# Performance work log

Measured on AMD Instinct MI355X. Metric: run time of the kernel, lower is better.

Reference implementation:

```python
import jax, jax.numpy as jnp
import numpy as np

B, D, E, H, DEPTH, NH, K = 4, 384, 8, 1536, 12, 6, 2
P, NTOK = 16, 197  # patch size, 14*14 patches + cls
EPS = 1e-6


def layernorm(x, w, b):
    m = x.mean(-1, keepdims=True)
    v = ((x - m) ** 2).mean(-1, keepdims=True)
    return (x - m) / jnp.sqrt(v + EPS) * w + b


def attention(x, qkv_w, qkv_b, proj_w, proj_b):
    Bn, N, C = x.shape
    hd = C // NH
    qkv = x @ qkv_w.T + qkv_b                       # [B,N,3C]
    qkv = qkv.reshape(Bn, N, 3, NH, hd).transpose(2, 0, 3, 1, 4)
    q, k, v = qkv[0], qkv[1], qkv[2]                # [B,h,N,hd]
    attn = jax.nn.softmax((q @ k.transpose(0, 1, 3, 2)) * (hd ** -0.5), axis=-1)
    out = (attn @ v).transpose(0, 2, 1, 3).reshape(Bn, N, C)
    return out @ proj_w.T + proj_b


def mlp(x, w1, b1, w2, b2):
    h = jax.nn.gelu(x @ w1.T + b1, approximate=False)
    return h @ w2.T + b2


def moe_ffn(x2d, gw, w1, b1, w2, b2):
    # noiseless top-k gating (eval mode of NoisyTopKGating)
    logits = x2d @ gw                                # [T,E]
    T = logits.shape[0]
    top_vals, top_idx = jax.lax.top_k(logits, K + 1)
    gates_k = jax.nn.softmax(top_vals[:, :K], axis=-1)
    gates = jnp.zeros((T, E), x2d.dtype).at[jnp.arange(T)[:, None], top_idx[:, :K]].set(gates_k)
    # dense per-expert FFN, weighted combine (identical math to SparseDispatcher)
    h = jax.nn.gelu(jnp.einsum('td,edh->teh', x2d, w1) + b1, approximate=False)
    out = jnp.einsum('teh,ehd->ted', h, w2) + b2
    return jnp.einsum('te,ted->td', gates, out)


def forward(x, patch_w, patch_b, cls_token, pos_embed,
            ln1_w, ln1_b, qkv_w, qkv_b, proj_w, proj_b, ln2_w, ln2_b,
            fc1_w, fc1_b, fc2_w, fc2_b,
            gate_w, moe_w1, moe_b1, moe_w2, moe_b2, lnf_w, lnf_b):
    # patch embed: conv k=16 s=16
    feat = jax.lax.conv_general_dilated(x, patch_w, (P, P), 'VALID',
                                        dimension_numbers=('NCHW', 'OIHW', 'NCHW'))
    feat = feat + patch_b[None, :, None, None]
    Bn = feat.shape[0]
    tokens = feat.reshape(Bn, D, -1).transpose(0, 2, 1)          # [B,196,D]
    cls = jnp.broadcast_to(cls_token, (Bn, 1, D))
    h = jnp.concatenate([cls, tokens], axis=1) + pos_embed       # [B,197,D]

    for i in range(DEPTH):
        h = h + attention(layernorm(h, ln1_w[i], ln1_b[i]), qkv_w[i], qkv_b[i], proj_w[i], proj_b[i])
        y = layernorm(h, ln2_w[i], ln2_b[i])
        if i % 2 == 1:
            j = i // 2
            y2 = moe_ffn(y.reshape(-1, D), gate_w[j], moe_w1[j], moe_b1[j], moe_w2[j], moe_b2[j])
            h = h + y2.reshape(Bn, NTOK, D)
        else:
            j = i // 2
            h = h + mlp(y, fc1_w[j], fc1_b[j], fc2_w[j], fc2_b[j])
    return layernorm(h, lnf_w, lnf_b)


def setup_inputs() -> dict:
    key = jax.random.key(0)
    ks = jax.random.split(key, 16)
    rn = lambda k, s, sd=0.02: jax.random.normal(k, s, jnp.float32) * sd
    return {
        'x': jax.random.normal(ks[0], (B, 3, 224, 224), jnp.float32),
        'patch_w': rn(ks[1], (D, 3, P, P)), 'patch_b': jnp.zeros((D,), jnp.float32),
        'cls_token': rn(ks[2], (1, 1, D)), 'pos_embed': rn(ks[3], (1, NTOK, D)),
        'ln1_w': jnp.ones((DEPTH, D), jnp.float32), 'ln1_b': jnp.zeros((DEPTH, D), jnp.float32),
        'qkv_w': rn(ks[4], (DEPTH, 3 * D, D)), 'qkv_b': jnp.zeros((DEPTH, 3 * D), jnp.float32),
        'proj_w': rn(ks[5], (DEPTH, D, D)), 'proj_b': jnp.zeros((DEPTH, D), jnp.float32),
        'ln2_w': jnp.ones((DEPTH, D), jnp.float32), 'ln2_b': jnp.zeros((DEPTH, D), jnp.float32),
        'fc1_w': rn(ks[6], (DEPTH // 2, H, D)), 'fc1_b': jnp.zeros((DEPTH // 2, H), jnp.float32),
        'fc2_w': rn(ks[7], (DEPTH // 2, D, H)), 'fc2_b': jnp.zeros((DEPTH // 2, D), jnp.float32),
        'gate_w': rn(ks[8], (DEPTH // 2, D, E)),
        'moe_w1': rn(ks[9], (DEPTH // 2, E, D, H)), 'moe_b1': jnp.zeros((DEPTH // 2, E, H), jnp.float32),
        'moe_w2': rn(ks[10], (DEPTH // 2, E, H, D)), 'moe_b2': jnp.zeros((DEPTH // 2, E, D), jnp.float32),
        'lnf_w': jnp.ones((D,), jnp.float32), 'lnf_b': jnp.zeros((D,), jnp.float32),
    }


def reference(x, patch_w, patch_b, cls_token, pos_embed,
              ln1_w, ln1_b, qkv_w, qkv_b, proj_w, proj_b, ln2_w, ln2_b,
              fc1_w, fc1_b, fc2_w, fc2_b,
              gate_w, moe_w1, moe_b1, moe_w2, moe_b2, lnf_w, lnf_b):
    return forward(x, patch_w, patch_b, cls_token, pos_embed,
                   ln1_w, ln1_b, qkv_w, qkv_b, proj_w, proj_b, ln2_w, ln2_b,
                   fc1_w, fc1_b, fc2_w, fc2_b,
                   gate_w, moe_w1, moe_b1, moe_w2, moe_b2, lnf_w, lnf_b)
```

## Files before the change

### kernel.cpp

```cpp
#include <hip/hip_runtime.h>
#include <math.h>

#define NBATCH 4
#define NTOK 197
#define TT 788
#define DM 384
#define HM 1536
#define NHEAD 6
#define NEXP 8
#define LD2 72
#define MOUTSZ (TT * 2 * DM)

typedef __attribute__((ext_vector_type(8))) short bf16x8;
typedef __attribute__((ext_vector_type(4))) float f32x4;

__device__ __forceinline__ void f2bf2(float x, short& hi, short& lo) {
    unsigned u = __float_as_uint(x);
    unsigned uh = u + (0x7fffu + ((u >> 16) & 1u));
    hi = (short)(uh >> 16);
    float hf = __uint_as_float(uh & 0xffff0000u);
    float r = x - hf;
    unsigned v = __float_as_uint(r);
    lo = (short)((v + (0x7fffu + ((v >> 16) & 1u))) >> 16);
}
__device__ __forceinline__ float gelu_f(float x) {
    return 0.5f * x * (1.0f + erff(x * 0.7071067811865475f));
}

__global__ void k_im2col(const float* __restrict__ X, float* __restrict__ P) {
    int p = blockIdx.x;
    int b = p / 196, pp = p % 196;
    int py = pp / 14, px = pp % 14;
    const float* xb = X + (size_t)b * 3 * 224 * 224;
    float* dst = P + (size_t)p * 768;
    for (int idx = threadIdx.x; idx < 768; idx += 256) {
        int c = idx >> 8;
        int i = (idx >> 4) & 15;
        int j = idx & 15;
        dst[idx] = xb[((size_t)c * 224 + py * 16 + i) * 224 + px * 16 + j];
    }
}

__global__ void k_assemble(const float* __restrict__ PO, const float* __restrict__ pb,
                           const float* __restrict__ cls, const float* __restrict__ pos,
                           float* __restrict__ H) {
    int t = blockIdx.x;
    int b = t / NTOK, n = t % NTOK;
    for (int d = threadIdx.x; d < DM; d += 128) {
        float v;
        if (n == 0) v = cls[d];
        else v = PO[((size_t)b * 196 + (n - 1)) * DM + d] + pb[d];
        H[(size_t)t * DM + d] = v + pos[(size_t)n * DM + d];
    }
}

__global__ void k_ln(const float* __restrict__ X, const float* __restrict__ w,
                     const float* __restrict__ b, float* __restrict__ Y) {
    int t = blockIdx.x, lane = threadIdx.x;
    const float* x = X + (size_t)t * DM;
    float v[6];
    float s = 0.f;
    #pragma unroll
    for (int i = 0; i < 6; ++i) { v[i] = x[lane + i * 64]; s += v[i]; }
    #pragma unroll
    for (int off = 32; off; off >>= 1) s += __shfl_xor(s, off);
    float mean = s * (1.f / 384.f);
    float q = 0.f;
    #pragma unroll
    for (int i = 0; i < 6; ++i) { float d = v[i] - mean; q += d * d; }
    #pragma unroll
    for (int off = 32; off; off >>= 1) q += __shfl_xor(q, off);
    float inv = rsqrtf(q * (1.f / 384.f) + 1e-6f);
    float* y = Y + (size_t)t * DM;
    #pragma unroll
    for (int i = 0; i < 6; ++i) {
        int d = lane + i * 64;
        y[d] = (v[i] - mean) * inv * w[d] + b[d];
    }
}

__global__ __launch_bounds__(256) void k_gemm_mfma(
    const float* __restrict__ A, const float* __restrict__ W,
    const float* __restrict__ bias, float* __restrict__ C,
    int M, int N, int K, int flags, int MT, int NT, int wprot,
    const float* __restrict__ lnw, const float* __restrict__ lnb)
{
    int mt, nt;
    {
        int lane8 = blockIdx.x & 7;
        int idx = blockIdx.x >> 3;
        if (wprot) {
            mt = idx % MT;
            nt = lane8 + 8 * (idx / MT);
            if (nt >= NT) return;
        } else {
            nt = idx % NT;
            mt = lane8 + 8 * (idx / NT);
            if (mt >= MT) return;
        }
    }
    __shared__ short Ah[64 * LD2], Al[64 * LD2], Bh[64 * LD2], Bl[64 * LD2];
    const int bm = mt * 64, bn = nt * 64;
    const int tid = threadIdx.x;
    const int lane = tid & 63, w = tid >> 6;
    const int wr = w >> 1, wc = w & 1;
    const int r16 = lane & 15, g = lane >> 4;
    const int sr = tid >> 4;
    const int sc = (tid & 15) * 4;
    const bool doln = (flags & 8) != 0;
    float am[4], ai[4];
    #pragma unroll
    for (int p = 0; p < 4; ++p) { am[p] = 0.f; ai[p] = 1.f; }
    if (doln) {
        int j = tid & 15;
        #pragma unroll
        for (int p = 0; p < 4; ++p) {
            int r = bm + sr + p * 16;
            if (r < M) {
                const float* xr = A + (size_t)r * K;
                float s = 0.f, ss = 0.f;
                #pragma unroll
                for (int i = 0; i < 6; ++i) {
                    float4 v = *(const float4*)(xr + j * 4 + i * 64);
                    s += v.x + v.y + v.z + v.w;
                    ss += v.x * v.x + v.y * v.y + v.z * v.z + v.w * v.w;
                }
                #pragma unroll
                for (int off = 1; off < 16; off <<= 1) {
                    s += __shfl_xor(s, off);
                    ss += __shfl_xor(ss, off);
                }
                float mean = s * (1.f / 384.f);
                float var = ss * (1.f / 384.f) - mean * mean;
                am[p] = mean;
                ai[p] = rsqrtf(var + 1e-6f);
            }
        }
    }
    float4 ra[4], rb[4], lw4, lb4;
    auto LOADT = [&](int k0) {
        if (doln) {
            lw4 = *(const float4*)(lnw + k0 + sc);
            lb4 = *(const float4*)(lnb + k0 + sc);
        }
        #pragma unroll
        for (int p = 0; p < 4; ++p) {
            int r = sr + p * 16;
            ra[p] = make_float4(0.f, 0.f, 0.f, 0.f);
            if (bm + r < M) ra[p] = *(const float4*)(A + (size_t)(bm + r) * K + k0 + sc);
            rb[p] = *(const float4*)(W + (size_t)(bn + r) * K + k0 + sc);
        }
    };
    auto STORET = [&]() {
        #pragma unroll
        for (int p = 0; p < 4; ++p) {
            int r = sr + p * 16;
            float4 a4 = ra[p];
            if (doln) {
                a4.x = (a4.x - am[p]) * ai[p] * lw4.x + lb4.x;
                a4.y = (a4.y - am[p]) * ai[p] * lw4.y + lb4.y;
                a4.z = (a4.z - am[p]) * ai[p] * lw4.z + lb4.z;
                a4.w = (a4.w - am[p]) * ai[p] * lw4.w + lb4.w;
            }
            float4 b4 = rb[p];
            short4 ah, al, bh, bl;
            f2bf2(a4.x, ah.x, al.x); f2bf2(a4.y, ah.y, al.y);
            f2bf2(a4.z, ah.z, al.z); f2bf2(a4.w, ah.w, al.w);
            f2bf2(b4.x, bh.x, bl.x); f2bf2(b4.y, bh.y, bl.y);
            f2bf2(b4.z, bh.z, bl.z); f2bf2(b4.w, bh.w, bl.w);
            *(short4*)&Ah[r * LD2 + sc] = ah; *(short4*)&Al[r * LD2 + sc] = al;
            *(short4*)&Bh[r * LD2 + sc] = bh; *(short4*)&Bl[r * LD2 + sc] = bl;
        }
    };
    f32x4 acc[2][2] = {};
    auto COMPUTE = [&]() {
        #pragma unroll
        for (int kk = 0; kk < 2; ++kk) {
            bf16x8 afh[2], afl[2], bfh[2], bfl[2];
            #pragma unroll
            for (int i = 0; i < 2; ++i) {
                int off = (wr * 32 + i * 16 + r16) * LD2 + kk * 32 + g * 8;
                afh[i] = *(const bf16x8*)&Ah[off];
                afl[i] = *(const bf16x8*)&Al[off];
            }
            #pragma unroll
            for (int j = 0; j < 2; ++j) {
                int off = (wc * 32 + j * 16 + r16) * LD2 + kk * 32 + g * 8;
                bfh[j] = *(const bf16x8*)&Bh[off];
                bfl[j] = *(const bf16x8*)&Bl[off];
            }
            #pragma unroll
            for (int i = 0; i < 2; ++i)
                #pragma unroll
                for (int j = 0; j < 2; ++j) {
                    acc[i][j] = __builtin_amdgcn_mfma_f32_16x16x32_bf16(afl[i], bfh[j], acc[i][j], 0, 0, 0);
                    acc[i][j] = __builtin_amdgcn_mfma_f32_16x16x32_bf16(afh[i], bfl[j], acc[i][j], 0, 0, 0);
                    acc[i][j] = __builtin_amdgcn_mfma_f32_16x16x32_bf16(afh[i], bfh[j], acc[i][j], 0, 0, 0);
                }
        }
    };
    LOADT(0);
    STORET();
    __syncthreads();
    for (int k0 = 64; k0 < K; k0 += 64) {
        LOADT(k0);
        COMPUTE();
        __syncthreads();
        STORET();
        __syncthreads();
    }
    COMPUTE();
    #pragma unroll
    for (int i = 0; i < 2; ++i) {
        #pragma unroll
        for (int j = 0; j < 2; ++j) {
            int n = bn + wc * 32 + j * 16 + r16;
            float bb = bias ? bias[n] : 0.f;
            int mbase = bm + wr * 32 + i * 16 + g * 4;
            #pragma unroll
            for (int r = 0; r < 4; ++r) {
                int m = mbase + r;
                if (m < M) {
                    float v = acc[i][j][r] + bb;
                    if (flags & 1) v = gelu_f(v);
                    float* cp = C + (size_t)m * N + n;
                    if (flags & 2) v += *cp;
                    *cp = v;
                }
            }
        }
    }
}

__global__ __launch_bounds__(256) void k_scoresm(const float* __restrict__ QKV,
                                                 float* __restrict__ S) {
    int z = blockIdx.y;
    int b = z / NHEAD, hh = z % NHEAD;
    int i0 = blockIdx.x * 32;
    __shared__ float qs[32][65];
    __shared__ float ks[32][65];
    __shared__ float srow[32][200];
    int tid = threadIdx.x;
    int r = tid >> 3, d0 = (tid & 7) * 8, c0 = (tid & 7) * 4, l8 = tid & 7;
    {
        float4 v0 = make_float4(0,0,0,0), v1 = v0;
        if (i0 + r < NTOK) {
            const float* qp = QKV + ((size_t)(b * NTOK + i0 + r)) * 1152 + hh * 64 + d0;
            v0 = *(const float4*)qp; v1 = *(const float4*)(qp + 4);
        }
        qs[r][d0+0]=v0.x; qs[r][d0+1]=v0.y; qs[r][d0+2]=v0.z; qs[r][d0+3]=v0.w;
        qs[r][d0+4]=v1.x; qs[r][d0+5]=v1.y; qs[r][d0+6]=v1.z; qs[r][d0+7]=v1.w;
    }
    if (l8 == 0) { srow[r][197] = -1e30f; srow[r][198] = -1e30f; srow[r][199] = -1e30f; }
    for (int j0 = 0; j0 < NTOK; j0 += 32) {
        __syncthreads();
        {
            float4 v0 = make_float4(0,0,0,0), v1 = v0;
            if (j0 + r < NTOK) {
                const float* kp = QKV + ((size_t)(b * NTOK + j0 + r)) * 1152 + 384 + hh * 64 + d0;
                v0 = *(const float4*)kp; v1 = *(const float4*)(kp + 4);
            }
            ks[r][d0+0]=v0.x; ks[r][d0+1]=v0.y; ks[r][d0+2]=v0.z; ks[r][d0+3]=v0.w;
            ks[r][d0+4]=v1.x; ks[r][d0+5]=v1.y; ks[r][d0+6]=v1.z; ks[r][d0+7]=v1.w;
        }
        __syncthreads();
        float acc[4] = {0.f, 0.f, 0.f, 0.f};
        #pragma unroll 8
        for (int d = 0; d < 64; ++d) {
            float qv = qs[r][d];
            #pragma unroll
            for (int u = 0; u < 4; ++u) acc[u] += qv * ks[c0 + u][d];
        }
        #pragma unroll
        for (int u = 0; u < 4; ++u) {
            int j = j0 + c0 + u;
            if (j < NTOK) srow[r][j] = acc[u] * 0.125f;
        }
    }
    __syncthreads();
    float m = -1e30f;
    for (int c = l8; c < 200; c += 8) m = fmaxf(m, srow[r][c]);
    #pragma unroll
    for (int off = 1; off < 8; off <<= 1) m = fmaxf(m, __shfl_xor(m, off));
    float s = 0.f;
    for (int c = l8; c < 200; c += 8) {
        float e = expf(srow[r][c] - m);
        srow[r][c] = e;
        s += e;
    }
    #pragma unroll
    for (int off = 1; off < 8; off <<= 1) s += __shfl_xor(s, off);
    float invs = 1.f / s;
    int i = i0 + r;
    if (i < NTOK) {
        float* sp = S + ((size_t)z * NTOK + i) * NTOK;
        for (int c = l8; c < NTOK; c += 8) sp[c] = srow[r][c] * invs;
    }
}

__global__ __launch_bounds__(256) void k_pv(const float* __restrict__ S, const float* __restrict__ QKV,
                                            float* __restrict__ AO) {
    int z = blockIdx.y;
    int b = z / NHEAD, hh = z % NHEAD;
    int i0 = blockIdx.x * 32;
    __shared__ float ps[32][33];
    __shared__ float vs[32][65];
    int tid = threadIdx.x;
    int r = tid >> 3;
    int c4 = (tid & 7) * 4;
    int d0 = (tid & 7) * 8;
    float acc[8] = {};
    for (int k0 = 0; k0 < NTOK; k0 += 32) {
        #pragma unroll
        for (int u = 0; u < 4; ++u) {
            int i = i0 + r, j = k0 + c4 + u;
            ps[r][c4 + u] = (i < NTOK && j < NTOK) ? S[((size_t)z * NTOK + i) * NTOK + j] : 0.f;
        }
        {
            float4 v0 = make_float4(0,0,0,0), v1 = v0;
            if (k0 + r < NTOK) {
                const float* vp = QKV + ((size_t)(b * NTOK + k0 + r)) * 1152 + 768 + hh * 64 + d0;
                v0 = *(const float4*)vp; v1 = *(const float4*)(vp + 4);
            }
            vs[r][d0+0]=v0.x; vs[r][d0+1]=v0.y; vs[r][d0+2]=v0.z; vs[r][d0+3]=v0.w;
            vs[r][d0+4]=v1.x; vs[r][d0+5]=v1.y; vs[r][d0+6]=v1.z; vs[r][d0+7]=v1.w;
        }
        __syncthreads();
        #pragma unroll 8
        for (int kk = 0; kk < 32; ++kk) {
            float pw = ps[r][kk];
            #pragma unroll
            for (int j = 0; j < 8; ++j) acc[j] += pw * vs[kk][d0 + j];
        }
        __syncthreads();
    }
    int i = i0 + r;
    if (i < NTOK) {
        float* op = AO + (size_t)(b * NTOK + i) * DM + hh * 64 + d0;
        #pragma unroll
        for (int j = 0; j < 8; ++j) op[j] = acc[j];
    }
}

__global__ void k_route_ln(const float* __restrict__ H, float* __restrict__ lnstat,
                           const float* __restrict__ lnw, const float* __restrict__ lnb,
                           const float* __restrict__ GW,
                           int* __restrict__ eidx, float* __restrict__ egate) {
    int t = blockIdx.x * 4 + (threadIdx.x >> 6);
    if (t >= TT) return;
    int lane = threadIdx.x & 63;
    const float* x = H + (size_t)t * DM;
    float v[6];
    float s = 0.f, ss = 0.f;
    #pragma unroll
    for (int i = 0; i < 6; ++i) {
        v[i] = x[lane + i * 64];
        s += v[i];
        ss += v[i] * v[i];
    }
    #pragma unroll
    for (int off = 32; off; off >>= 1) { s += __shfl_xor(s, off); ss += __shfl_xor(ss, off); }
    float mean = s * (1.f / 384.f);
    float var = ss * (1.f / 384.f) - mean * mean;
    float inv = rsqrtf(var + 1e-6f);
    if (lane == 0) { lnstat[2 * t] = mean; lnstat[2 * t + 1] = inv; }
    float l8[NEXP] = {};
    #pragma unroll
    for (int i = 0; i < 6; ++i) {
        int d = lane + i * 64;
        float yv = (v[i] - mean) * inv * lnw[d] + lnb[d];
        const float* g = GW + (size_t)d * NEXP;
        #pragma unroll
        for (int e = 0; e < NEXP; ++e) l8[e] += yv * g[e];
    }
    #pragma unroll
    for (int e = 0; e < NEXP; ++e) {
        float vv = l8[e];
        #pragma unroll
        for (int off = 32; off; off >>= 1) vv += __shfl_xor(vv, off);
        l8[e] = vv;
    }
    if (lane == 0) {
        int b0 = 0;
        #pragma unroll
        for (int e = 1; e < NEXP; ++e) if (l8[e] > l8[b0]) b0 = e;
        int b1 = -1;
        #pragma unroll
        for (int e = 0; e < NEXP; ++e) if (e != b0 && (b1 < 0 || l8[e] > l8[b1])) b1 = e;
        float e1 = expf(l8[b1] - l8[b0]);
        float denom = 1.f + e1;
        eidx[2 * t] = b0; eidx[2 * t + 1] = b1;
        egate[2 * t] = 1.f / denom; egate[2 * t + 1] = e1 / denom;
    }
}

__global__ void k_pscatter(int* __restrict__ cnt, int* __restrict__ basep,
                           const int* __restrict__ eidx,
                           int* __restrict__ slot_tok, int* __restrict__ slot_of) {
    __shared__ int hist[NEXP];
    __shared__ int bp[NEXP];
    __shared__ int fl[NEXP];
    int tid = threadIdx.x;
    if (tid < NEXP) { hist[tid] = 0; fl[tid] = 0; }
    __syncthreads();
    for (int i = tid; i < 2 * TT; i += 256) atomicAdd(&hist[eidx[i]], 1);
    __syncthreads();
    if (tid == 0) {
        int s = 0;
        for (int e = 0; e < NEXP; ++e) { bp[e] = s; s += hist[e]; }
    }
    __syncthreads();
    if (tid < NEXP) { cnt[tid] = hist[tid]; basep[tid] = bp[tid]; }
    for (int t = tid; t < TT; t += 256) {
        #pragma unroll
        for (int k = 0; k < 2; ++k) {
            int e = eidx[2 * t + k];
            int pos = atomicAdd(&fl[e], 1);
            int s = bp[e] + pos;
            slot_tok[s] = t;
            slot_of[2 * t + k] = s;
        }
    }
}

__global__ __launch_bounds__(256) void k_moe1_mfma(
    const float* __restrict__ H, const float* __restrict__ lnstat,
    const float* __restrict__ lnw, const float* __restrict__ lnb,
    const float* __restrict__ W1, const float* __restrict__ B1,
    const int* __restrict__ slot_tok, const int* __restrict__ cnt, const int* __restrict__ basep,
    float* __restrict__ HID)
{
    const int e = blockIdx.x & 7;
    const int idx = blockIdx.x >> 3;
    const int mt = idx % 25;
    const int nt = idx / 25;
    const int c = cnt[e];
    const int r0 = mt * 64;
    if (r0 >= c) return;
    const int sbase = basep[e];
    const int n0 = nt * 64;
    const float* W = W1 + (size_t)e * DM * HM;
    const float* B1e = B1 + (size_t)e * HM;
    __shared__ short Ah[64 * LD2], Al[64 * LD2], Bh[64 * LD2], Bl[64 * LD2];
    const int tid = threadIdx.x;
    const int lane = tid & 63, w = tid >> 6;
    const int wr = w >> 1, wc = w & 1;
    const int r16 = lane & 15, g = lane >> 4;
    const int sr = tid >> 4, sc = (tid & 15) * 4;
    const int kq = (tid >> 4) * 4;
    int tokp[4];
    float am4[4], ai4[4];
    #pragma unroll
    for (int p = 0; p < 4; ++p) {
        int m = r0 + sr + p * 16;
        tokp[p] = (m < c) ? slot_tok[sbase + m] : -1;
        am4[p] = 0.f; ai4[p] = 1.f;
        if (tokp[p] >= 0) { am4[p] = lnstat[2 * tokp[p]]; ai4[p] = lnstat[2 * tokp[p] + 1]; }
    }
    f32x4 acc[2][2] = {};
    for (int k0 = 0; k0 < DM; k0 += 64) {
        float4 lw4 = *(const float4*)(lnw + k0 + sc);
        float4 lb4 = *(const float4*)(lnb + k0 + sc);
        #pragma unroll
        for (int p = 0; p < 4; ++p) {
            int r = sr + p * 16;
            float4 a4 = make_float4(0.f, 0.f, 0.f, 0.f);
            if (tokp[p] >= 0) {
                a4 = *(const float4*)(H + (size_t)tokp[p] * DM + k0 + sc);
                a4.x = (a4.x - am4[p]) * ai4[p] * lw4.x + lb4.x;
                a4.y = (a4.y - am4[p]) * ai4[p] * lw4.y + lb4.y;
                a4.z = (a4.z - am4[p]) * ai4[p] * lw4.z + lb4.z;
                a4.w = (a4.w - am4[p]) * ai4[p] * lw4.w + lb4.w;
            }
            short4 ah, al;
            f2bf2(a4.x, ah.x, al.x); f2bf2(a4.y, ah.y, al.y);
            f2bf2(a4.z, ah.z, al.z); f2bf2(a4.w, ah.w, al.w);
            *(short4*)&Ah[r * LD2 + sc] = ah; *(short4*)&Al[r * LD2 + sc] = al;
        }
        {
            float4 b4[4];
            #pragma unroll
            for (int i = 0; i < 4; ++i)
                b4[i] = *(const float4*)(W + (size_t)(k0 + kq + i) * HM + n0 + sc);
            float col[4][4] = {
                { b4[0].x, b4[1].x, b4[2].x, b4[3].x },
                { b4[0].y, b4[1].y, b4[2].y, b4[3].y },
                { b4[0].z, b4[1].z, b4[2].z, b4[3].z },
                { b4[0].w, b4[1].w, b4[2].w, b4[3].w } };
            #pragma unroll
            for (int u = 0; u < 4; ++u) {
                short4 hh, ll;
                f2bf2(col[u][0], hh.x, ll.x); f2bf2(col[u][1], hh.y, ll.y);
                f2bf2(col[u][2], hh.z, ll.z); f2bf2(col[u][3], hh.w, ll.w);
                *(short4*)&Bh[(sc + u) * LD2 + kq] = hh;
                *(short4*)&Bl[(sc + u) * LD2 + kq] = ll;
            }
        }
        __syncthreads();
        #pragma unroll
        for (int kk = 0; kk < 2; ++kk) {
            bf16x8 afh[2], afl[2], bfh[2], bfl[2];
            #pragma unroll
            for (int i = 0; i < 2; ++i) {
                int off = (wr * 32 + i * 16 + r16) * LD2 + kk * 32 + g * 8;
                afh[i] = *(const bf16x8*)&Ah[off];
                afl[i] = *(const bf16x8*)&Al[off];
            }
            #pragma unroll
            for (int j = 0; j < 2; ++j) {
                int off = (wc * 32 + j * 16 + r16) * LD2 + kk * 32 + g * 8;
                bfh[j] = *(const bf16x8*)&Bh[off];
                bfl[j] = *(const bf16x8*)&Bl[off];
            }
            #pragma unroll
            for (int i = 0; i < 2; ++i)
                #pragma unroll
                for (int j = 0; j < 2; ++j) {
                    acc[i][j] = __builtin_amdgcn_mfma_f32_16x16x32_bf16(afl[i], bfh[j], acc[i][j], 0, 0, 0);
                    acc[i][j] = __builtin_amdgcn_mfma_f32_16x16x32_bf16(afh[i], bfl[j], acc[i][j], 0, 0, 0);
                    acc[i][j] = __builtin_amdgcn_mfma_f32_16x16x32_bf16(afh[i], bfh[j], acc[i][j], 0, 0, 0);
                }
        }
        __syncthreads();
    }
    #pragma unroll
    for (int i = 0; i < 2; ++i) {
        #pragma unroll
        for (int j = 0; j < 2; ++j) {
            int n = n0 + wc * 32 + j * 16 + r16;
            float bb = B1e[n];
            #pragma unroll
            for (int r = 0; r < 4; ++r) {
                int m = r0 + wr * 32 + i * 16 + g * 4 + r;
                if (m < c)
                    HID[(size_t)(sbase + m) * HM + n] = gelu_f(acc[i][j][r] + bb);
            }
        }
    }
}

__global__ __launch_bounds__(256) void k_moe2_mfma(
    const float* __restrict__ HID, const float* __restrict__ W2,
    const int* __restrict__ cnt, const int* __restrict__ basep,
    float* __restrict__ MOUTP)
{
    const int e = blockIdx.x & 7;
    const int idx = blockIdx.x >> 3;
    const int mt = idx % 25;
    const int rest = idx / 25;
    const int nt = rest % 6;
    const int ks = rest / 6;
    const int c = cnt[e];
    const int r0 = mt * 64;
    if (r0 >= c) return;
    const int sbase = basep[e];
    const int n0 = nt * 64;
    const int kbase = ks * 384;
    const float* W = W2 + (size_t)e * HM * DM + (size_t)kbase * DM;
    float* outp = MOUTP + (size_t)ks * MOUTSZ;
    __shared__ short Ah[64 * LD2], Al[64 * LD2], Bh[64 * LD2], Bl[64 * LD2];
    const int tid = threadIdx.x;
    const int lane = tid & 63, w = tid >> 6;
    const int wr = w >> 1, wc = w & 1;
    const int r16 = lane & 15, g = lane >> 4;
    const int sr = tid >> 4, sc = (tid & 15) * 4;
    const int kq = (tid >> 4) * 4;
    f32x4 acc[2][2] = {};
    for (int k0 = 0; k0 < 384; k0 += 64) {
        #pragma unroll
        for (int p = 0; p < 4; ++p) {
            int r = sr + p * 16;
            int m = r0 + r;
            float4 a4 = make_float4(0.f, 0.f, 0.f, 0.f);
            if (m < c) a4 = *(const float4*)(HID + (size_t)(sbase + m) * HM + kbase + k0 + sc);
            short4 ah, al;
            f2bf2(a4.x, ah.x, al.x); f2bf2(a4.y, ah.y, al.y);
            f2bf2(a4.z, ah.z, al.z); f2bf2(a4.w, ah.w, al.w);
            *(short4*)&Ah[r * LD2 + sc] = ah; *(short4*)&Al[r * LD2 + sc] = al;
        }
        {
            float4 b4[4];
            #pragma unroll
            for (int i = 0; i < 4; ++i)
                b4[i] = *(const float4*)(W + (size_t)(k0 + kq + i) * DM + n0 + sc);
            float col[4][4] = {
                { b4[0].x, b4[1].x, b4[2].x, b4[3].x },
                { b4[0].y, b4[1].y, b4[2].y, b4[3].y },
                { b4[0].z, b4[1].z, b4[2].z, b4[3].z },
                { b4[0].w, b4[1].w, b4[2].w, b4[3].w } };
            #pragma unroll
            for (int u = 0; u < 4; ++u) {
                short4 hh, ll;
                f2bf2(col[u][0], hh.x, ll.x); f2bf2(col[u][1], hh.y, ll.y);
                f2bf2(col[u][2], hh.z, ll.z); f2bf2(col[u][3], hh.w, ll.w);
                *(short4*)&Bh[(sc + u) * LD2 + kq] = hh;
                *(short4*)&Bl[(sc + u) * LD2 + kq] = ll;
            }
        }
        __syncthreads();
        #pragma unroll
        for (int kk = 0; kk < 2; ++kk) {
            bf16x8 afh[2], afl[2], bfh[2], bfl[2];
            #pragma unroll
            for (int i = 0; i < 2; ++i) {
                int off = (wr * 32 + i * 16 + r16) * LD2 + kk * 32 + g * 8;
                afh[i] = *(const bf16x8*)&Ah[off];
                afl[i] = *(const bf16x8*)&Al[off];
            }
            #pragma unroll
            for (int j = 0; j < 2; ++j) {
                int off = (wc * 32 + j * 16 + r16) * LD2 + kk * 32 + g * 8;
                bfh[j] = *(const bf16x8*)&Bh[off];
                bfl[j] = *(const bf16x8*)&Bl[off];
            }
            #pragma unroll
            for (int i = 0; i < 2; ++i)
                #pragma unroll
                for (int j = 0; j < 2; ++j) {
                    acc[i][j] = __builtin_amdgcn_mfma_f32_16x16x32_bf16(afl[i], bfh[j], acc[i][j], 0, 0, 0);
                    acc[i][j] = __builtin_amdgcn_mfma_f32_16x16x32_bf16(afh[i], bfl[j], acc[i][j], 0, 0, 0);
                    acc[i][j] = __builtin_amdgcn_mfma_f32_16x16x32_bf16(afh[i], bfh[j], acc[i][j], 0, 0, 0);
                }
        }
        __syncthreads();
    }
    #pragma unroll
    for (int i = 0; i < 2; ++i) {
        #pragma unroll
        for (int j = 0; j < 2; ++j) {
            int n = n0 + wc * 32 + j * 16 + r16;
            #pragma unroll
            for (int r = 0; r < 4; ++r) {
                int m = r0 + wr * 32 + i * 16 + g * 4 + r;
                if (m < c)
                    outp[(size_t)(sbase + m) * DM + n] = acc[i][j][r];
            }
        }
    }
}

__global__ void k_combine(const float* __restrict__ MOUTP, const int* __restrict__ slot_of,
                          const int* __restrict__ eidx, const float* __restrict__ egate,
                          const float* __restrict__ B2, float* __restrict__ H) {
    int t = blockIdx.x;
    int s0 = slot_of[2 * t], s1 = slot_of[2 * t + 1];
    int e0 = eidx[2 * t], e1 = eidx[2 * t + 1];
    float g0 = egate[2 * t], g1 = egate[2 * t + 1];
    for (int d = threadIdx.x; d < DM; d += 128) {
        float v0 = B2[(size_t)e0 * DM + d];
        float v1 = B2[(size_t)e1 * DM + d];
        #pragma unroll
        for (int p = 0; p < 4; ++p) {
            v0 += MOUTP[(size_t)p * MOUTSZ + (size_t)s0 * DM + d];
            v1 += MOUTP[(size_t)p * MOUTSZ + (size_t)s1 * DM + d];
        }
        H[(size_t)t * DM + d] += g0 * v0 + g1 * v1;
    }
}

extern "C" void kernel_launch(void* const* d_in, const int* in_sizes, int n_in,
                              void* d_out, int out_size, void* d_ws, size_t ws_size,
                              hipStream_t stream) {
    const float* x         = (const float*)d_in[0];
    const float* patch_w   = (const float*)d_in[1];
    const float* patch_b   = (const float*)d_in[2];
    const float* cls_token = (const float*)d_in[3];
    const float* pos_embed = (const float*)d_in[4];
    const float* ln1_w     = (const float*)d_in[5];
    const float* ln1_b     = (const float*)d_in[6];
    const float* qkv_w     = (const float*)d_in[7];
    const float* qkv_b     = (const float*)d_in[8];
    const float* proj_w    = (const float*)d_in[9];
    const float* proj_b    = (const float*)d_in[10];
    const float* ln2_w     = (const float*)d_in[11];
    const float* ln2_b     = (const float*)d_in[12];
    const float* fc1_w     = (const float*)d_in[13];
    const float* fc1_b     = (const float*)d_in[14];
    const float* fc2_w     = (const float*)d_in[15];
    const float* fc2_b     = (const float*)d_in[16];
    const float* gate_w    = (const float*)d_in[17];
    const float* moe_w1    = (const float*)d_in[18];
    const float* moe_b1    = (const float*)d_in[19];
    const float* moe_w2    = (const float*)d_in[20];
    const float* moe_b2    = (const float*)d_in[21];
    const float* lnf_w     = (const float*)d_in[22];
    const float* lnf_b     = (const float*)d_in[23];
    float* out = (float*)d_out;

    float* wsf = (float*)d_ws;
    float* regA     = wsf;
    float* patches  = regA;
    float* patchout = regA + 602112;
    float* moehid   = regA;
    float* h     = regA + 2420736;
    float* spare = h + 302592;
    float* qkvb  = spare + 302592;
    float* attno = qkvb + 907776;
    float* regC  = attno + 302592;
    float* S    = regC;
    float* hid  = regC;
    float* mout4 = qkvb;
    float* egate = regC + 1210368;
    int* ib       = (int*)(egate + 1576);
    int* eidx     = ib;
    int* slot_tok = ib + 1576;
    int* slot_of  = ib + 3152;
    int* cnt      = ib + 4728;
    int* basep    = ib + 4736;
    float* lnstat = (float*)(ib + 4752);

    k_im2col<<<784, 256, 0, stream>>>(x, patches);
    k_gemm_mfma<<<96, 256, 0, stream>>>(patches, patch_w, nullptr, patchout,
                                        784, DM, 768, 0, 13, 6, 0, nullptr, nullptr);
    k_assemble<<<TT, 128, 0, stream>>>(patchout, patch_b, cls_token, pos_embed, h);

    for (int l = 0; l < 12; ++l) {
        k_gemm_mfma<<<312, 256, 0, stream>>>(h, qkv_w + (size_t)l * 1152 * DM,
                                             qkv_b + l * 1152, qkvb, TT, 1152, DM, 8,
                                             13, 18, 1,
                                             ln1_w + l * DM, ln1_b + l * DM);
        k_scoresm<<<dim3(7, NBATCH * NHEAD), 256, 0, stream>>>(qkvb, S);
        k_pv<<<dim3(7, NBATCH * NHEAD), 256, 0, stream>>>(S, qkvb, attno);
        k_gemm_mfma<<<96, 256, 0, stream>>>(attno, proj_w + (size_t)l * DM * DM,
                                            proj_b + l * DM, h, TT, DM, DM, 2,
                                            13, 6, 0, nullptr, nullptr);
        int j = l >> 1;
        if ((l & 1) == 0) {
            k_gemm_mfma<<<312, 256, 0, stream>>>(h, fc1_w + (size_t)j * HM * DM,
                                                 fc1_b + j * HM, hid, TT, HM, DM, 9,
                                                 13, 24, 1,
                                                 ln2_w + l * DM, ln2_b + l * DM);
            k_gemm_mfma<<<96, 256, 0, stream>>>(hid, fc2_w + (size_t)j * DM * HM,
                                                fc2_b + j * DM, h, TT, DM, HM, 2,
                                                13, 6, 0, nullptr, nullptr);
        } else {
            k_route_ln<<<197, 256, 0, stream>>>(h, lnstat, ln2_w + l * DM, ln2_b + l * DM,
                                                gate_w + (size_t)j * DM * NEXP, eidx, egate);
            k_pscatter<<<1, 256, 0, stream>>>(cnt, basep, eidx, slot_tok, slot_of);
            k_moe1_mfma<<<8 * 25 * 24, 256, 0, stream>>>(
                h, lnstat, ln2_w + l * DM, ln2_b + l * DM,
                moe_w1 + (size_t)j * NEXP * DM * HM, moe_b1 + (size_t)j * NEXP * HM,
                slot_tok, cnt, basep, moehid);
            k_moe2_mfma<<<8 * 25 * 24, 256, 0, stream>>>(
                moehid, moe_w2 + (size_t)j * NEXP * HM * DM, cnt, basep, mout4);
            k_combine<<<TT, 128, 0, stream>>>(mout4, slot_of, eidx, egate,
                                              moe_b2 + (size_t)j * NEXP * DM, h);
        }
    }
    k_ln<<<TT, 64, 0, stream>>>(h, lnf_w, lnf_b, out);
}
```

Before: 1.787 ms.

## Add split-K with atomic accumulation for proj/fc2 GEMMs and trim MoE grids

Adds a ksplit parameter to the MFMA GEMM so the projection and fc2 GEMMs split K across 2 and 4 blocks. Each slice adds its partial result straight into the residual h with atomicAdd, and only slice 0 adds the bias. This raises those launches from 96 blocks to 192/384 so more of the GPU is busy. It also shrinks the MoE kernels' m-tile count per expert from 25 to 13, which still covers the at most 788 slots per expert while launching fewer blocks that exit at once. The cost is atomic traffic, non-deterministic summation order, and redundant A/W reads per K-slice.

```diff
diff --git a/kernel.cpp b/kernel.cpp
--- a/kernel.cpp
+++ b/kernel.cpp
@@ -82,13 +82,14 @@
 __global__ __launch_bounds__(256) void k_gemm_mfma(
     const float* __restrict__ A, const float* __restrict__ W,
     const float* __restrict__ bias, float* __restrict__ C,
-    int M, int N, int K, int flags, int MT, int NT, int wprot,
+    int M, int N, int K, int flags, int MT, int NT, int wprot, int ksplit,
     const float* __restrict__ lnw, const float* __restrict__ lnb)
 {
-    int mt, nt;
+    int mt, nt, ks = 0;
     {
         int lane8 = blockIdx.x & 7;
         int idx = blockIdx.x >> 3;
+        if (ksplit > 1) { ks = idx % ksplit; idx /= ksplit; }
         if (wprot) {
             mt = idx % MT;
             nt = lane8 + 8 * (idx / MT);
@@ -99,6 +100,9 @@
             if (mt >= MT) return;
         }
     }
+    const int Ks = K / ksplit;
+    const float* Ab = A + (size_t)ks * Ks;
+    const float* Wb = W + (size_t)ks * Ks;
     __shared__ short Ah[64 * LD2], Al[64 * LD2], Bh[64 * LD2], Bl[64 * LD2];
     const int bm = mt * 64, bn = nt * 64;
     const int tid = threadIdx.x;
@@ -147,8 +151,8 @@
         for (int p = 0; p < 4; ++p) {
             int r = sr + p * 16;
             ra[p] = make_float4(0.f, 0.f, 0.f, 0.f);
-            if (bm + r < M) ra[p] = *(const float4*)(A + (size_t)(bm + r) * K + k0 + sc);
-            rb[p] = *(const float4*)(W + (size_t)(bn + r) * K + k0 + sc);
+            if (bm + r < M) ra[p] = *(const float4*)(Ab + (size_t)(bm + r) * K + k0 + sc);
+            rb[p] = *(const float4*)(Wb + (size_t)(bn + r) * K + k0 + sc);
         }
     };
     auto STORET = [&]() {
@@ -202,7 +206,7 @@
     LOADT(0);
     STORET();
     __syncthreads();
-    for (int k0 = 64; k0 < K; k0 += 64) {
+    for (int k0 = 64; k0 < Ks; k0 += 64) {
         LOADT(k0);
         COMPUTE();
         __syncthreads();
@@ -215,17 +219,21 @@
         #pragma unroll
         for (int j = 0; j < 2; ++j) {
             int n = bn + wc * 32 + j * 16 + r16;
-            float bb = bias ? bias[n] : 0.f;
+            float bb = (bias && ks == 0) ? bias[n] : 0.f;
             int mbase = bm + wr * 32 + i * 16 + g * 4;
             #pragma unroll
             for (int r = 0; r < 4; ++r) {
                 int m = mbase + r;
                 if (m < M) {
                     float v = acc[i][j][r] + bb;
-                    if (flags & 1) v = gelu_f(v);
                     float* cp = C + (size_t)m * N + n;
-                    if (flags & 2) v += *cp;
-                    *cp = v;
+                    if (flags & 16) {
+                        atomicAdd(cp, v);
+                    } else {
+                        if (flags & 1) v = gelu_f(v);
+                        if (flags & 2) v += *cp;
+                        *cp = v;
+                    }
                 }
             }
         }
@@ -364,30 +372,30 @@
     float var = ss * (1.f / 384.f) - mean * mean;
     float inv = rsqrtf(var + 1e-6f);
     if (lane == 0) { lnstat[2 * t] = mean; lnstat[2 * t + 1] = inv; }
-    float l8[NEXP] = {};
+    float l8v[NEXP] = {};
     #pragma unroll
     for (int i = 0; i < 6; ++i) {
         int d = lane + i * 64;
         float yv = (v[i] - mean) * inv * lnw[d] + lnb[d];
         const float* g = GW + (size_t)d * NEXP;
         #pragma unroll
-        for (int e = 0; e < NEXP; ++e) l8[e] += yv * g[e];
+        for (int e = 0; e < NEXP; ++e) l8v[e] += yv * g[e];
     }
     #pragma unroll
     for (int e = 0; e < NEXP; ++e) {
-        float vv = l8[e];
+        float vv = l8v[e];
         #pragma unroll
         for (int off = 32; off; off >>= 1) vv += __shfl_xor(vv, off);
-        l8[e] = vv;
+        l8v[e] = vv;
     }
     if (lane == 0) {
         int b0 = 0;
         #pragma unroll
-        for (int e = 1; e < NEXP; ++e) if (l8[e] > l8[b0]) b0 = e;
+        for (int e = 1; e < NEXP; ++e) if (l8v[e] > l8v[b0]) b0 = e;
         int b1 = -1;
         #pragma unroll
-        for (int e = 0; e < NEXP; ++e) if (e != b0 && (b1 < 0 || l8[e] > l8[b1])) b1 = e;
-        float e1 = expf(l8[b1] - l8[b0]);
+        for (int e = 0; e < NEXP; ++e) if (e != b0 && (b1 < 0 || l8v[e] > l8v[b1])) b1 = e;
+        float e1 = expf(l8v[b1] - l8v[b0]);
         float denom = 1.f + e1;
         eidx[2 * t] = b0; eidx[2 * t + 1] = b1;
         egate[2 * t] = 1.f / denom; egate[2 * t + 1] = e1 / denom;
@@ -432,8 +440,8 @@
 {
     const int e = blockIdx.x & 7;
     const int idx = blockIdx.x >> 3;
-    const int mt = idx % 25;
-    const int nt = idx / 25;
+    const int mt = idx % 13;
+    const int nt = idx / 13;
     const int c = cnt[e];
     const int r0 = mt * 64;
     if (r0 >= c) return;
@@ -546,8 +554,8 @@
 {
     const int e = blockIdx.x & 7;
     const int idx = blockIdx.x >> 3;
-    const int mt = idx % 25;
-    const int rest = idx / 25;
+    const int mt = idx % 13;
+    const int rest = idx / 13;
     const int nt = rest % 6;
     const int ks = rest / 6;
     const int c = cnt[e];
@@ -711,37 +719,37 @@
 
     k_im2col<<<784, 256, 0, stream>>>(x, patches);
     k_gemm_mfma<<<96, 256, 0, stream>>>(patches, patch_w, nullptr, patchout,
-                                        784, DM, 768, 0, 13, 6, 0, nullptr, nullptr);
+                                        784, DM, 768, 0, 13, 6, 0, 1, nullptr, nullptr);
     k_assemble<<<TT, 128, 0, stream>>>(patchout, patch_b, cls_token, pos_embed, h);
 
     for (int l = 0; l < 12; ++l) {
         k_gemm_mfma<<<312, 256, 0, stream>>>(h, qkv_w + (size_t)l * 1152 * DM,
                                              qkv_b + l * 1152, qkvb, TT, 1152, DM, 8,
-                                             13, 18, 1,
+                                             13, 18, 1, 1,
                                              ln1_w + l * DM, ln1_b + l * DM);
         k_scoresm<<<dim3(7, NBATCH * NHEAD), 256, 0, stream>>>(qkvb, S);
         k_pv<<<dim3(7, NBATCH * NHEAD), 256, 0, stream>>>(S, qkvb, attno);
-        k_gemm_mfma<<<96, 256, 0, stream>>>(attno, proj_w + (size_t)l * DM * DM,
-                                            proj_b + l * DM, h, TT, DM, DM, 2,
-                                            13, 6, 0, nullptr, nullptr);
+        k_gemm_mfma<<<192, 256, 0, stream>>>(attno, proj_w + (size_t)l * DM * DM,
+                                             proj_b + l * DM, h, TT, DM, DM, 16,
+                                             13, 6, 0, 2, nullptr, nullptr);
         int j = l >> 1;
         if ((l & 1) == 0) {
             k_gemm_mfma<<<312, 256, 0, stream>>>(h, fc1_w + (size_t)j * HM * DM,
                                                  fc1_b + j * HM, hid, TT, HM, DM, 9,
-                                                 13, 24, 1,
+                                                 13, 24, 1, 1,
                                                  ln2_w + l * DM, ln2_b + l * DM);
-            k_gemm_mfma<<<96, 256, 0, stream>>>(hid, fc2_w + (size_t)j * DM * HM,
-                                                fc2_b + j * DM, h, TT, DM, HM, 2,
-                                                13, 6, 0, nullptr, nullptr);
+            k_gemm_mfma<<<384, 256, 0, stream>>>(hid, fc2_w + (size_t)j * DM * HM,
+                                                 fc2_b + j * DM, h, TT, DM, HM, 16,
+                                                 13, 6, 0, 4, nullptr, nullptr);
         } else {
             k_route_ln<<<197, 256, 0, stream>>>(h, lnstat, ln2_w + l * DM, ln2_b + l * DM,
                                                 gate_w + (size_t)j * DM * NEXP, eidx, egate);
             k_pscatter<<<1, 256, 0, stream>>>(cnt, basep, eidx, slot_tok, slot_of);
-            k_moe1_mfma<<<8 * 25 * 24, 256, 0, stream>>>(
+            k_moe1_mfma<<<8 * 13 * 24, 256, 0, stream>>>(
                 h, lnstat, ln2_w + l * DM, ln2_b + l * DM,
                 moe_w1 + (size_t)j * NEXP * DM * HM, moe_b1 + (size_t)j * NEXP * HM,
                 slot_tok, cnt, basep, moehid);
-            k_moe2_mfma<<<8 * 25 * 24, 256, 0, stream>>>(
+            k_moe2_mfma<<<8 * 13 * 24, 256, 0, stream>>>(
                 moehid, moe_w2 + (size_t)j * NEXP * HM * DM, cnt, basep, mout4);
             k_combine<<<TT, 128, 0, stream>>>(mout4, slot_of, eidx, egate,
                                               moe_b2 + (size_t)j * NEXP * DM, h);
```

After: 1.669 ms, median of 2. 1.07x faster.
